# Performance work log

Measured on AMD Instinct MI355X. Metric: run time of the kernel, lower is better.

Reference implementation:

```python
import jax, jax.numpy as jnp
import numpy as np

F_ = 16      # features
H = 256      # hidden_features
C = 256      # context_features
L = 12       # num_layers
K = 16       # num_bins
M = 3 * K - 1  # output dim multiplier per feature (widths K, heights K, derivs K-1)
TB = 3.0     # tail_bound
MINW = 1e-3  # min bin width/height (nflows defaults)
MIND = 1e-3  # min derivative


def _masks():
    # nflows MADE sequential degrees
    in_deg = np.arange(1, F_ + 1)
    hid_deg = np.arange(H) % (F_ - 1) + 1
    m0 = (hid_deg[:, None] >= in_deg[None, :]).astype(np.float32)   # [H,F] initial layer
    mh = (hid_deg[:, None] >= hid_deg[None, :]).astype(np.float32)  # [H,H] hidden layers
    out_deg = np.repeat(in_deg, M)                                   # nflows tile = repeat_interleave
    mf = (out_deg[:, None] > hid_deg[None, :]).astype(np.float32)   # [F*M,H] output layer (strict)
    return jnp.asarray(m0), jnp.asarray(mh), jnp.asarray(mf)


def _made(x, ctx, W0, b0, Wc, bc, Wr, br, Wf, bf, m0, mh, mf):
    # MADE with 2 masked residual blocks, relu, context injected at initial layer
    h = x @ (W0 * m0).T + b0 + ctx @ Wc.T + bc
    for blk in range(2):
        t = jax.nn.relu(h) @ (Wr[blk, 0] * mh).T + br[blk, 0]
        t = jax.nn.relu(t) @ (Wr[blk, 1] * mh).T + br[blk, 1]
        h = h + t
    return h @ (Wf * mf).T + bf  # [B, F*M]


def _rq_spline(x, uw, uh, ud):
    # unconstrained rational-quadratic spline with linear tails (nflows math)
    inside = (x >= -TB) & (x <= TB)
    xc = jnp.clip(x, -TB, TB)
    const = float(np.log(np.expm1(1.0 - MIND)))
    ud = jnp.pad(ud, ((0, 0), (0, 0), (1, 1)), constant_values=const)  # edge derivs -> 1
    w = MINW + (1 - MINW * K) * jax.nn.softmax(uw, axis=-1)
    cw = jnp.pad(jnp.cumsum(w, -1), ((0, 0), (0, 0), (1, 0)))
    cw = (2 * TB * cw - TB).at[..., 0].set(-TB).at[..., -1].set(TB)
    w = cw[..., 1:] - cw[..., :-1]
    hgt = MINW + (1 - MINW * K) * jax.nn.softmax(uh, axis=-1)
    ch = jnp.pad(jnp.cumsum(hgt, -1), ((0, 0), (0, 0), (1, 0)))
    ch = (2 * TB * ch - TB).at[..., 0].set(-TB).at[..., -1].set(TB)
    hgt = ch[..., 1:] - ch[..., :-1]
    d = MIND + jax.nn.softplus(ud)  # [B,F,K+1]
    locs = cw.at[..., -1].add(1e-6)
    idx = jnp.clip(jnp.sum((xc[..., None] >= locs).astype(jnp.int32), -1) - 1, 0, K - 1)[..., None]
    g = lambda a: jnp.take_along_axis(a, idx, -1)[..., 0]
    icw, iw, ich, ih = g(cw), g(w), g(ch), g(hgt)
    delta = ih / iw
    dk = g(d)
    dk1 = jnp.take_along_axis(d, idx + 1, -1)[..., 0]
    th = (xc - icw) / iw
    t1m = th * (1 - th)
    den = delta + (dk + dk1 - 2 * delta) * t1m
    y = ich + ih * (delta * th ** 2 + dk * t1m) / den
    dnum = delta ** 2 * (dk1 * th ** 2 + 2 * delta * t1m + dk * (1 - th) ** 2)
    ld = jnp.log(dnum) - 2 * jnp.log(den)
    return jnp.where(inside, y, x), jnp.where(inside, ld, 0.0)


def _forward(x, context, W0, b0, Wc, bc, Wr, br, Wf, bf):
    m0, mh, mf = _masks()
    B = x.shape[0]
    logdet = jnp.zeros((B,), x.dtype)
    s = 1.0 / np.sqrt(H)  # nflows divides widths/heights by sqrt(hidden_features)
    for l in range(L):
        x = x[:, ::-1]  # ReversePermutation (logdet 0)
        p = _made(x, context, W0[l], b0[l], Wc[l], bc[l], Wr[l], br[l], Wf[l], bf[l], m0, mh, mf)
        p = p.reshape(B, F_, M)
        x, ld = _rq_spline(x, p[..., :K] * s, p[..., K:2 * K] * s, p[..., 2 * K:])
        logdet = logdet + ld.sum(-1)
    return x, logdet


def setup_inputs() -> dict:
    key = jax.random.key(0)
    ks = jax.random.split(key, 8)
    B = 65536
    x = jax.random.normal(ks[0], (B, F_), dtype=jnp.float32)
    context = jax.random.normal(ks[1], (B, C), dtype=jnp.float32)
    W0 = jax.random.normal(ks[2], (L, H, F_), dtype=jnp.float32) / np.sqrt(F_)
    b0 = jnp.zeros((L, H), jnp.float32)
    Wc = jax.random.normal(ks[3], (L, H, C), dtype=jnp.float32) / np.sqrt(C)
    bc = jnp.zeros((L, H), jnp.float32)
    Wr = jax.random.normal(ks[4], (L, 2, 2, H, H), dtype=jnp.float32) / np.sqrt(H)
    br = jnp.zeros((L, 2, 2, H), jnp.float32)
    Wf = jax.random.normal(ks[5], (L, F_ * M, H), dtype=jnp.float32) / np.sqrt(H)
    bf = jnp.zeros((L, F_ * M), jnp.float32)
    return {"x": x, "context": context, "W0": W0, "b0": b0, "Wc": Wc, "bc": bc,
            "Wr": Wr, "br": br, "Wf": Wf, "bf": bf}


def reference(x, context, W0, b0, Wc, bc, Wr, br, Wf, bf):
    return _forward(x, context, W0, b0, Wc, bc, Wr, br, Wf, bf)
```

## Files before the change

kernel.cpp:

```cpp
#include <hip/hip_runtime.h>

typedef _Float16 f16_t;
typedef _Float16 f16x8 __attribute__((ext_vector_type(8)));
typedef _Float16 f16x4 __attribute__((ext_vector_type(4)));
typedef _Float16 f16x2 __attribute__((ext_vector_type(2)));
typedef float    f32x4 __attribute__((ext_vector_type(4)));

#define LAYERS 12
#define HDIM   256
#define CDIM   256
#define BROWS  32

#define W0P_OFF 0
#define WCP_OFF 8192
#define WRP_OFF 73728
#define WRP_SZ  65536
#define WFP_OFF 335872
#define LSTRIDE 532480
#define PACK_TOTAL (LAYERS * LSTRIDE)
#define CTX_BYTE ((size_t)PACK_TOTAL * 2)

#define WAIT_VM(N)  __builtin_amdgcn_s_waitcnt(0x0F70 | (N))
#define WAIT_LGKM0  __builtin_amdgcn_s_waitcnt(0xC07F)

__global__ __launch_bounds__(256) void nsf_pack(
    const float* __restrict__ W0, const float* __restrict__ Wc,
    const float* __restrict__ Wr, const float* __restrict__ Wf,
    f16_t* __restrict__ wp)
{
    int e = blockIdx.x * 256 + threadIdx.x;
    if (e >= PACK_TOTAL) return;
    int l = e / LSTRIDE;
    int r = e - l * LSTRIDE;
    float v = 0.f;
    if (r < WCP_OFF) {
        int t = r >> 9, lane = (r >> 3) & 63, j = r & 7;
        int n = t * 16 + (lane & 15);
        int k = (lane >> 4) * 8 + j;
        if (k < 16 && (n % 15 + 1) >= (k + 1))
            v = W0[(l * HDIM + n) * 16 + k];
    } else if (r < WRP_OFF) {
        int q = r - WCP_OFF;
        int t = q >> 9, lane = (q >> 3) & 63, j = q & 7;
        int n = (t >> 3) * 16 + (lane & 15);
        int k = (t & 7) * 32 + (lane >> 4) * 8 + j;
        v = Wc[(l * HDIM + n) * CDIM + k];
    } else if (r < WFP_OFF) {
        int q = r - WRP_OFF;
        int rr = q >> 16; q &= 65535;
        int t = q >> 9, lane = (q >> 3) & 63, j = q & 7;
        int n = (t >> 3) * 16 + (lane & 15);
        int k = (t & 7) * 32 + (lane >> 4) * 8 + j;
        if ((n % 15) >= (k % 15))
            v = Wr[(((l * 2 + (rr >> 1)) * 2 + (rr & 1)) * HDIM + n) * HDIM + k];
    } else {
        int q = r - WFP_OFF;
        int t = q >> 9, lane = (q >> 3) & 63, j = q & 7;
        int np = (t >> 3) * 16 + (lane & 15);
        int k = (t & 7) * 32 + (lane >> 4) * 8 + j;
        int f = np / 48, jj = np % 48;
        if (jj < 47 && (f + 1) > (k % 15 + 1))
            v = Wf[(l * 752 + f * 47 + jj) * HDIM + k];
    }
    wp[e] = (f16_t)v;
}

__global__ __launch_bounds__(256) void nsf_ctx16(
    const float* __restrict__ ctx, f16_t* __restrict__ c16, int n4)
{
    int i = blockIdx.x * 256 + threadIdx.x;
    if (i >= n4) return;
    float4 v = reinterpret_cast<const float4*>(ctx)[i];
    f16x4 o = { (f16_t)v.x, (f16_t)v.y, (f16_t)v.z, (f16_t)v.w };
    reinterpret_cast<f16x4*>(c16)[i] = o;
}

__device__ __forceinline__ float splus(float x) {
    return fmaxf(x, 0.f) + __logf(1.f + __expf(-fabsf(x)));
}
__device__ __forceinline__ float loF(unsigned u) {
    f16x2 h = __builtin_bit_cast(f16x2, u); return (float)h[0];
}
__device__ __forceinline__ float hiF(unsigned u) {
    f16x2 h = __builtin_bit_cast(f16x2, u); return (float)h[1];
}

__device__ __forceinline__ void load_lds16(const f16_t* g, f16_t* l) {
    __builtin_amdgcn_global_load_lds(
        (const __attribute__((address_space(1))) void*)(g),
        (__attribute__((address_space(3))) void*)(l), 16, 0, 0);
}

__device__ __forceinline__ void issue4(const f16_t* gbase, f16_t* slot, int kt) {
#pragma unroll
    for (int ni = 0; ni < 4; ++ni)
        load_lds16(gbase + ni * 4096 + kt * 512, slot + ni * 512);
}
__device__ __forceinline__ void issue3(const f16_t* gbase, f16_t* slot, int kt) {
#pragma unroll
    for (int ni = 0; ni < 3; ++ni)
        load_lds16(gbase + ni * 4096 + kt * 512, slot + ni * 512);
}

__device__ __forceinline__ void gemm256_lds(f32x4 (&acc)[2][4],
                                            const f16_t (&A)[BROWS][264],
                                            const f16_t* __restrict__ wb,
                                            f16_t* s0, f16_t* s1,
                                            int wave, int lane, int quad, int l16)
{
    const f16_t* gbase = wb + (size_t)wave * 4 * 4096 + lane * 8;
    issue4(gbase, s0, 0);
    issue4(gbase, s1, 1);
#pragma unroll
    for (int kt = 0; kt < 8; ++kt) {
        f16_t* cs = (kt & 1) ? s1 : s0;
        if (kt < 7) WAIT_VM(4); else WAIT_VM(0);
        f16x8 b[4];
#pragma unroll
        for (int ni = 0; ni < 4; ++ni)
            b[ni] = *reinterpret_cast<const f16x8*>(cs + ni * 512 + lane * 8);
        f16x8 a[2];
#pragma unroll
        for (int mi = 0; mi < 2; ++mi)
            a[mi] = *reinterpret_cast<const f16x8*>(&A[mi * 16 + l16][kt * 32 + quad * 8]);
#pragma unroll
        for (int ni = 0; ni < 4; ++ni)
#pragma unroll
            for (int mi = 0; mi < 2; ++mi)
                acc[mi][ni] = __builtin_amdgcn_mfma_f32_16x16x32_f16(a[mi], b[ni], acc[mi][ni], 0, 0, 0);
        if (kt < 6) { WAIT_LGKM0; issue4(gbase, cs, kt + 2); }
    }
}

template <bool RELU>
__device__ __forceinline__ void stage_c(const f32x4 (&acc)[2][4], f16_t (&A)[BROWS][264],
                                        int wave, int quad, int l16)
{
#pragma unroll
    for (int mi = 0; mi < 2; ++mi)
#pragma unroll
        for (int ni = 0; ni < 4; ++ni)
#pragma unroll
            for (int rr = 0; rr < 4; ++rr) {
                float v = acc[mi][ni][rr];
                if (RELU) v = fmaxf(v, 0.f);
                A[mi * 16 + quad * 4 + rr][wave * 64 + ni * 16 + l16] = (f16_t)v;
            }
}

template <bool CTX16>
__global__ __launch_bounds__(256, 2)
void nsf_flow(
    const float* __restrict__ x_in, const float* __restrict__ ctx32,
    const f16_t* __restrict__ ctx16,
    const float* __restrict__ b0, const float* __restrict__ bc,
    const float* __restrict__ br, const float* __restrict__ bfb,
    const f16_t* __restrict__ wp,
    float* __restrict__ out, int B)
{
    __shared__ f16_t act[BROWS][264];
    __shared__ __align__(16) f16_t wbuf[4][2][2048];
    __shared__ f16_t pldsw[4][32][50];
    __shared__ f16_t xstage[BROWS][40];
    __shared__ float xbuf[BROWS][16];
    __shared__ float ldsum[32][4];

    const int tid  = threadIdx.x;
    const int wave = tid >> 6, lane = tid & 63;
    const int quad = lane >> 4, l16 = lane & 15;
    const int row0 = blockIdx.x * BROWS;

    f16_t* s0 = &wbuf[wave][0][0];
    f16_t* s1 = &wbuf[wave][1][0];

    for (int i = tid; i < BROWS * 16; i += 256)
        xbuf[i >> 4][i & 15] = x_in[(size_t)row0 * 16 + i];

    float ld_acc = 0.f;

#pragma unroll 1
    for (int l = 0; l < LAYERS; ++l) {
        const f16_t* wl = wp + (size_t)l * LSTRIDE;
        __syncthreads();

        float xval_c[4];
        if (lane < 32) {
#pragma unroll
            for (int c = 0; c < 4; ++c) xval_c[c] = xbuf[lane][15 - (wave * 4 + c)];
        }

        if (CTX16) {
#pragma unroll
            for (int it = 0; it < 4; ++it) {
                int j = it * 256 + tid;
                int rr = j >> 5, cg = j & 31;
                f16x8 v = *reinterpret_cast<const f16x8*>(ctx16 + (size_t)(row0 + rr) * CDIM + cg * 8);
                *reinterpret_cast<f16x8*>(&act[rr][cg * 8]) = v;
            }
        } else {
            int rr = tid >> 3, cg = tid & 7;
            const float* cptr = ctx32 + (size_t)(row0 + rr) * CDIM + cg * 32;
#pragma unroll
            for (int it = 0; it < 8; ++it) {
                float4 v = *reinterpret_cast<const float4*>(cptr + it * 4);
                f16x4 w4 = { (f16_t)v.x, (f16_t)v.y, (f16_t)v.z, (f16_t)v.w };
                *reinterpret_cast<f16x4*>(&act[rr][cg * 32 + it * 4]) = w4;
            }
        }
        for (int i = tid; i < BROWS * 32; i += 256) {
            int rr = i >> 5, c = i & 31;
            float v = (c < 16) ? xbuf[rr][15 - c] : 0.f;
            xstage[rr][c] = (f16_t)v;
        }
        __syncthreads();

        f32x4 hacc[2][4];
#pragma unroll
        for (int ni = 0; ni < 4; ++ni) {
            int n = wave * 64 + ni * 16 + l16;
            float bv = b0[l * HDIM + n] + bc[l * HDIM + n];
#pragma unroll
            for (int mi = 0; mi < 2; ++mi) hacc[mi][ni] = (f32x4){bv, bv, bv, bv};
        }
        {
            f16x8 a[2];
#pragma unroll
            for (int mi = 0; mi < 2; ++mi)
                a[mi] = *reinterpret_cast<const f16x8*>(&xstage[mi * 16 + l16][quad * 8]);
#pragma unroll
            for (int ni = 0; ni < 4; ++ni) {
                f16x8 b = *reinterpret_cast<const f16x8*>(wl + W0P_OFF + ((wave * 4 + ni) * 64 + lane) * 8);
#pragma unroll
                for (int mi = 0; mi < 2; ++mi)
                    hacc[mi][ni] = __builtin_amdgcn_mfma_f32_16x16x32_f16(a[mi], b, hacc[mi][ni], 0, 0, 0);
            }
        }
        gemm256_lds(hacc, act, wl + WCP_OFF, s0, s1, wave, lane, quad, l16);

#pragma unroll 1
        for (int blk = 0; blk < 2; ++blk) {
            __syncthreads();
            stage_c<true>(hacc, act, wave, quad, l16);
            __syncthreads();
            f32x4 tacc[2][4];
#pragma unroll
            for (int ni = 0; ni < 4; ++ni) {
                int n = wave * 64 + ni * 16 + l16;
                float bv = br[((l * 2 + blk) * 2 + 0) * HDIM + n];
#pragma unroll
                for (int mi = 0; mi < 2; ++mi) tacc[mi][ni] = (f32x4){bv, bv, bv, bv};
            }
            gemm256_lds(tacc, act, wl + WRP_OFF + (size_t)(blk * 2) * WRP_SZ, s0, s1, wave, lane, quad, l16);
            __syncthreads();
            stage_c<true>(tacc, act, wave, quad, l16);
            __syncthreads();
#pragma unroll
            for (int ni = 0; ni < 4; ++ni) {
                int n = wave * 64 + ni * 16 + l16;
                float bv = br[((l * 2 + blk) * 2 + 1) * HDIM + n];
#pragma unroll
                for (int mi = 0; mi < 2; ++mi) tacc[mi][ni] = (f32x4){bv, bv, bv, bv};
            }
            gemm256_lds(tacc, act, wl + WRP_OFF + (size_t)(blk * 2 + 1) * WRP_SZ, s0, s1, wave, lane, quad, l16);
#pragma unroll
            for (int mi = 0; mi < 2; ++mi)
#pragma unroll
                for (int ni = 0; ni < 4; ++ni)
                    hacc[mi][ni] += tacc[mi][ni];
        }

        __syncthreads();
        stage_c<false>(hacc, act, wave, quad, l16);
        __syncthreads();

#pragma unroll 1
        for (int c = 0; c < 4; ++c) {
            const int f = wave * 4 + c;
            const f16_t* gbase = wl + WFP_OFF + (size_t)(3 * f) * 4096 + lane * 8;
            f32x4 pacc[2][3];
#pragma unroll
            for (int ni = 0; ni < 3; ++ni) {
                int jj = ni * 16 + l16;
                float bv = (jj < 47) ? bfb[l * 752 + f * 47 + jj] : 0.f;
#pragma unroll
                for (int mi = 0; mi < 2; ++mi) pacc[mi][ni] = (f32x4){bv, bv, bv, bv};
            }
            issue3(gbase, s0, 0);
            issue3(gbase, s1, 1);
#pragma unroll
            for (int kt = 0; kt < 8; ++kt) {
                f16_t* cs = (kt & 1) ? s1 : s0;
                if (kt < 7) WAIT_VM(3); else WAIT_VM(0);
                f16x8 b[3];
#pragma unroll
                for (int ni = 0; ni < 3; ++ni)
                    b[ni] = *reinterpret_cast<const f16x8*>(cs + ni * 512 + lane * 8);
                f16x8 a[2];
#pragma unroll
                for (int mi = 0; mi < 2; ++mi)
                    a[mi] = *reinterpret_cast<const f16x8*>(&act[mi * 16 + l16][kt * 32 + quad * 8]);
#pragma unroll
                for (int ni = 0; ni < 3; ++ni)
#pragma unroll
                    for (int mi = 0; mi < 2; ++mi)
                        pacc[mi][ni] = __builtin_amdgcn_mfma_f32_16x16x32_f16(a[mi], b[ni], pacc[mi][ni], 0, 0, 0);
                if (kt < 6) { WAIT_LGKM0; issue3(gbase, cs, kt + 2); }
            }
            WAIT_LGKM0;
#pragma unroll
            for (int mi = 0; mi < 2; ++mi)
#pragma unroll
                for (int ni = 0; ni < 3; ++ni)
#pragma unroll
                    for (int rr = 0; rr < 4; ++rr)
                        pldsw[wave][mi * 16 + quad * 4 + rr][ni * 16 + l16] = (f16_t)pacc[mi][ni][rr];
            WAIT_LGKM0;

            if (lane < 32) {
                float xval = xval_c[c];
                const unsigned* pp = reinterpret_cast<const unsigned*>(&pldsw[wave][lane][0]);
                float uw[16], uh[16], ud[15];
#pragma unroll
                for (int j = 0; j < 8; ++j) {
                    unsigned w2 = pp[j], h2 = pp[8 + j];
                    uw[2 * j]     = loF(w2) * 0.0625f;
                    uw[2 * j + 1] = hiF(w2) * 0.0625f;
                    uh[2 * j]     = loF(h2) * 0.0625f;
                    uh[2 * j + 1] = hiF(h2) * 0.0625f;
                }
#pragma unroll
                for (int j = 0; j < 7; ++j) {
                    unsigned d2 = pp[16 + j];
                    ud[2 * j]     = loF(d2);
                    ud[2 * j + 1] = hiF(d2);
                }
                ud[14] = loF(pp[23]);

                float mw = uw[0], mh2 = uh[0];
#pragma unroll
                for (int j = 1; j < 16; ++j) { mw = fmaxf(mw, uw[j]); mh2 = fmaxf(mh2, uh[j]); }
                float sw = 0.f, sh = 0.f;
#pragma unroll
                for (int j = 0; j < 16; ++j) {
                    uw[j] = __expf(uw[j] - mw); sw += uw[j];
                    uh[j] = __expf(uh[j] - mh2); sh += uh[j];
                }
                float rw = 0.984f / sw, rh = 0.984f / sh;
                float xc = fminf(fmaxf(xval, -3.f), 3.f);
                float cumw = 0.f, cumh = 0.f, dprev = 1.f;
                float icw = -3.f, iwv = 1.f, ich = -3.f, ihv = 1.f, dk = 1.f, dk1 = 1.f;
#pragma unroll
                for (int j = 0; j < 16; ++j) {
                    float wj = fmaf(rw, uw[j], 0.001f);
                    float hj = fmaf(rh, uh[j], 0.001f);
                    float cwn = cumw + wj, chn = cumh + hj;
                    float left  = (j == 0)  ? -3.f : fmaf(6.f, cumw, -3.f);
                    float right = (j == 15) ?  3.f : fmaf(6.f, cwn, -3.f);
                    float hl    = (j == 0)  ? -3.f : fmaf(6.f, cumh, -3.f);
                    float hr    = (j == 15) ?  3.f : fmaf(6.f, chn, -3.f);
                    float dn    = (j == 15) ? 1.f : (0.001f + splus(ud[j]));
                    if (xc >= left) {
                        icw = left; iwv = right - left;
                        ich = hl;   ihv = hr - hl;
                        dk = dprev; dk1 = dn;
                    }
                    cumw = cwn; cumh = chn; dprev = dn;
                }
                float delta = ihv / iwv;
                float th = (xc - icw) / iwv;
                float omth = 1.f - th;
                float t1m = th * omth;
                float den = delta + (dk + dk1 - 2.f * delta) * t1m;
                float y = ich + ihv * (delta * th * th + dk * t1m) / den;
                float dnum = delta * delta * (dk1 * th * th + 2.f * delta * t1m + dk * omth * omth);
                float ldv = __logf(dnum) - 2.f * __logf(den);
                bool inside = (xval >= -3.f) && (xval <= 3.f);
                xbuf[lane][f] = inside ? y : xval;
                ld_acc += inside ? ldv : 0.f;
            }
        }
    }

    __syncthreads();
    for (int i = tid; i < BROWS * 16; i += 256)
        out[(size_t)row0 * 16 + i] = xbuf[i >> 4][i & 15];
    if (lane < 32) ldsum[lane][wave] = ld_acc;
    __syncthreads();
    if (tid < 32)
        out[(size_t)B * 16 + row0 + tid] =
            ldsum[tid][0] + ldsum[tid][1] + ldsum[tid][2] + ldsum[tid][3];
}

extern "C" void kernel_launch(void* const* d_in, const int* in_sizes, int n_in,
                              void* d_out, int out_size, void* d_ws, size_t ws_size,
                              hipStream_t stream)
{
    const float* x   = (const float*)d_in[0];
    const float* ctx = (const float*)d_in[1];
    const float* W0  = (const float*)d_in[2];
    const float* b0  = (const float*)d_in[3];
    const float* Wc  = (const float*)d_in[4];
    const float* bc  = (const float*)d_in[5];
    const float* Wr  = (const float*)d_in[6];
    const float* br  = (const float*)d_in[7];
    const float* Wf  = (const float*)d_in[8];
    const float* bfb = (const float*)d_in[9];
    int B = in_sizes[0] / 16;

    f16_t* wp  = (f16_t*)d_ws;
    f16_t* c16 = (f16_t*)((char*)d_ws + CTX_BYTE);
    bool useCtx16 = ws_size >= CTX_BYTE + (size_t)B * CDIM * 2;

    nsf_pack<<<(PACK_TOTAL + 255) / 256, 256, 0, stream>>>(W0, Wc, Wr, Wf, wp);
    if (useCtx16) {
        int n4 = B * CDIM / 4;
        nsf_ctx16<<<(n4 + 255) / 256, 256, 0, stream>>>(ctx, c16, n4);
        nsf_flow<true><<<B / BROWS, 256, 0, stream>>>(x, ctx, c16, b0, bc, br, bfb, wp, (float*)d_out, B);
    } else {
        nsf_flow<false><<<B / BROWS, 256, 0, stream>>>(x, ctx, c16, b0, bc, br, bfb, wp, (float*)d_out, B);
    }
}
```

Before: 1.902 ms.

## Load weight fragments directly to registers instead of staging through LDS

Result: faster. 1.586 ms (-16.6%).

```diff
diff --git a/kernel.cpp b/kernel.cpp
--- a/kernel.cpp
+++ b/kernel.cpp
@@ -20,7 +20,6 @@
 #define PACK_TOTAL (LAYERS * LSTRIDE)
 #define CTX_BYTE ((size_t)PACK_TOTAL * 2)
 
-#define WAIT_VM(N)  __builtin_amdgcn_s_waitcnt(0x0F70 | (N))
 #define WAIT_LGKM0  __builtin_amdgcn_s_waitcnt(0xC07F)
 
 __global__ __launch_bounds__(256) void nsf_pack(
@@ -85,50 +84,27 @@
     f16x2 h = __builtin_bit_cast(f16x2, u); return (float)h[1];
 }
 
-__device__ __forceinline__ void load_lds16(const f16_t* g, f16_t* l) {
-    __builtin_amdgcn_global_load_lds(
-        (const __attribute__((address_space(1))) void*)(g),
-        (__attribute__((address_space(3))) void*)(l), 16, 0, 0);
-}
-
-__device__ __forceinline__ void issue4(const f16_t* gbase, f16_t* slot, int kt) {
-#pragma unroll
-    for (int ni = 0; ni < 4; ++ni)
-        load_lds16(gbase + ni * 4096 + kt * 512, slot + ni * 512);
-}
-__device__ __forceinline__ void issue3(const f16_t* gbase, f16_t* slot, int kt) {
-#pragma unroll
-    for (int ni = 0; ni < 3; ++ni)
-        load_lds16(gbase + ni * 4096 + kt * 512, slot + ni * 512);
-}
-
-__device__ __forceinline__ void gemm256_lds(f32x4 (&acc)[2][4],
+template <int NT>
+__device__ __forceinline__ void gemm256_reg(f32x4 (&acc)[2][NT],
                                             const f16_t (&A)[BROWS][264],
-                                            const f16_t* __restrict__ wb,
-                                            f16_t* s0, f16_t* s1,
-                                            int wave, int lane, int quad, int l16)
-{
-    const f16_t* gbase = wb + (size_t)wave * 4 * 4096 + lane * 8;
-    issue4(gbase, s0, 0);
-    issue4(gbase, s1, 1);
+                                            const f16_t* __restrict__ gbase,
+                                            int quad, int l16)
+{
 #pragma unroll
     for (int kt = 0; kt < 8; ++kt) {
-        f16_t* cs = (kt & 1) ? s1 : s0;
-        if (kt < 7) WAIT_VM(4); else WAIT_VM(0);
-        f16x8 b[4];
-#pragma unroll
-        for (int ni = 0; ni < 4; ++ni)
-            b[ni] = *reinterpret_cast<const f16x8*>(cs + ni * 512 + lane * 8);
+        f16x8 b[NT];
+#pragma unroll
+        for (int ni = 0; ni < NT; ++ni)
+            b[ni] = *reinterpret_cast<const f16x8*>(gbase + ni * 4096 + kt * 512);
         f16x8 a[2];
 #pragma unroll
         for (int mi = 0; mi < 2; ++mi)
             a[mi] = *reinterpret_cast<const f16x8*>(&A[mi * 16 + l16][kt * 32 + quad * 8]);
 #pragma unroll
-        for (int ni = 0; ni < 4; ++ni)
+        for (int ni = 0; ni < NT; ++ni)
 #pragma unroll
             for (int mi = 0; mi < 2; ++mi)
                 acc[mi][ni] = __builtin_amdgcn_mfma_f32_16x16x32_f16(a[mi], b[ni], acc[mi][ni], 0, 0, 0);
-        if (kt < 6) { WAIT_LGKM0; issue4(gbase, cs, kt + 2); }
     }
 }
 
@@ -149,7 +125,7 @@
 }
 
 template <bool CTX16>
-__global__ __launch_bounds__(256, 2)
+__global__ __launch_bounds__(256, 4)
 void nsf_flow(
     const float* __restrict__ x_in, const float* __restrict__ ctx32,
     const f16_t* __restrict__ ctx16,
@@ -159,7 +135,6 @@
     float* __restrict__ out, int B)
 {
     __shared__ f16_t act[BROWS][264];
-    __shared__ __align__(16) f16_t wbuf[4][2][2048];
     __shared__ f16_t pldsw[4][32][50];
     __shared__ f16_t xstage[BROWS][40];
     __shared__ float xbuf[BROWS][16];
@@ -169,9 +144,6 @@
     const int wave = tid >> 6, lane = tid & 63;
     const int quad = lane >> 4, l16 = lane & 15;
     const int row0 = blockIdx.x * BROWS;
-
-    f16_t* s0 = &wbuf[wave][0][0];
-    f16_t* s1 = &wbuf[wave][1][0];
 
     for (int i = tid; i < BROWS * 16; i += 256)
         xbuf[i >> 4][i & 15] = x_in[(size_t)row0 * 16 + i];
@@ -235,7 +207,7 @@
                     hacc[mi][ni] = __builtin_amdgcn_mfma_f32_16x16x32_f16(a[mi], b, hacc[mi][ni], 0, 0, 0);
             }
         }
-        gemm256_lds(hacc, act, wl + WCP_OFF, s0, s1, wave, lane, quad, l16);
+        gemm256_reg<4>(hacc, act, wl + WCP_OFF + (size_t)wave * 4 * 4096 + lane * 8, quad, l16);
 
 #pragma unroll 1
         for (int blk = 0; blk < 2; ++blk) {
@@ -250,7 +222,8 @@
 #pragma unroll
                 for (int mi = 0; mi < 2; ++mi) tacc[mi][ni] = (f32x4){bv, bv, bv, bv};
             }
-            gemm256_lds(tacc, act, wl + WRP_OFF + (size_t)(blk * 2) * WRP_SZ, s0, s1, wave, lane, quad, l16);
+            gemm256_reg<4>(tacc, act,
+                wl + WRP_OFF + (size_t)(blk * 2) * WRP_SZ + (size_t)wave * 4 * 4096 + lane * 8, quad, l16);
             __syncthreads();
             stage_c<true>(tacc, act, wave, quad, l16);
             __syncthreads();
@@ -261,7 +234,8 @@
 #pragma unroll
                 for (int mi = 0; mi < 2; ++mi) tacc[mi][ni] = (f32x4){bv, bv, bv, bv};
             }
-            gemm256_lds(tacc, act, wl + WRP_OFF + (size_t)(blk * 2 + 1) * WRP_SZ, s0, s1, wave, lane, quad, l16);
+            gemm256_reg<4>(tacc, act,
+                wl + WRP_OFF + (size_t)(blk * 2 + 1) * WRP_SZ + (size_t)wave * 4 * 4096 + lane * 8, quad, l16);
 #pragma unroll
             for (int mi = 0; mi < 2; ++mi)
 #pragma unroll
@@ -276,7 +250,6 @@
 #pragma unroll 1
         for (int c = 0; c < 4; ++c) {
             const int f = wave * 4 + c;
-            const f16_t* gbase = wl + WFP_OFF + (size_t)(3 * f) * 4096 + lane * 8;
             f32x4 pacc[2][3];
 #pragma unroll
             for (int ni = 0; ni < 3; ++ni) {
@@ -285,28 +258,8 @@
 #pragma unroll
                 for (int mi = 0; mi < 2; ++mi) pacc[mi][ni] = (f32x4){bv, bv, bv, bv};
             }
-            issue3(gbase, s0, 0);
-            issue3(gbase, s1, 1);
-#pragma unroll
-            for (int kt = 0; kt < 8; ++kt) {
-                f16_t* cs = (kt & 1) ? s1 : s0;
-                if (kt < 7) WAIT_VM(3); else WAIT_VM(0);
-                f16x8 b[3];
-#pragma unroll
-                for (int ni = 0; ni < 3; ++ni)
-                    b[ni] = *reinterpret_cast<const f16x8*>(cs + ni * 512 + lane * 8);
-                f16x8 a[2];
-#pragma unroll
-                for (int mi = 0; mi < 2; ++mi)
-                    a[mi] = *reinterpret_cast<const f16x8*>(&act[mi * 16 + l16][kt * 32 + quad * 8]);
-#pragma unroll
-                for (int ni = 0; ni < 3; ++ni)
-#pragma unroll
-                    for (int mi = 0; mi < 2; ++mi)
-                        pacc[mi][ni] = __builtin_amdgcn_mfma_f32_16x16x32_f16(a[mi], b[ni], pacc[mi][ni], 0, 0, 0);
-                if (kt < 6) { WAIT_LGKM0; issue3(gbase, cs, kt + 2); }
-            }
-            WAIT_LGKM0;
+            gemm256_reg<3>(pacc, act, wl + WFP_OFF + (size_t)(3 * f) * 4096 + lane * 8, quad, l16);
+
 #pragma unroll
             for (int mi = 0; mi < 2; ++mi)
 #pragma unroll
```
